# Kernel optimization log

Measured on AMD Instinct MI355X. Metric: run time of the kernel, lower is better.

The kernel has to match this reference:

```python
import jax, jax.numpy as jnp
import numpy as np

V = 25426          # tgt_vocab_size
D = 256            # d_model
H = 8              # heads
DH = 2048          # dim_head (d_ff passed positionally as d_head in source)
INNER = H * DH     # 16384
CLS = V            # cls token id (same value for t1 and t2 in source)
MASK_TOK = V + 2   # mask token id
VT = V + 3         # total embedding vocab


def _pos_encoding(n, d):
    pos = np.arange(n, dtype=np.float32)[:, None]
    div = np.exp(np.arange(0, d, 2, dtype=np.float32) * (-np.log(10000.0) / d))
    pe = np.zeros((n, d), dtype=np.float32)
    pe[:, 0::2] = np.sin(pos * div)
    pe[:, 1::2] = np.cos(pos * div)
    return jnp.asarray(pe)


def _layernorm(x, g, b, eps=1e-5):
    m = x.mean(-1, keepdims=True)
    v = ((x - m) ** 2).mean(-1, keepdims=True)
    return (x - m) / jnp.sqrt(v + eps) * g + b


def _cross_attn(x, ctx, pad_mask, Wq, Wk, Wv, Wo, bo):
    # x: [B,N,D], ctx: [B,M,Dc], pad_mask: [B,M] True = masked
    B, N, _ = x.shape
    M = ctx.shape[1]
    scale = DH ** -0.5
    q = (x @ Wq).reshape(B, N, H, DH)
    k = (ctx @ Wk).reshape(B, M, H, DH)
    v = (ctx @ Wv).reshape(B, M, H, DH)
    sim = jnp.einsum('bihd,bjhd->bhij', q, k) * scale  # [B,H,N,M]
    neg = -jnp.finfo(sim.dtype).max
    sim = jnp.where(pad_mask[:, None, None, :], neg, sim)
    attn = jax.nn.softmax(sim, axis=-1)
    out = jnp.einsum('bhij,bjhd->bihd', attn, v).reshape(B, N, INNER)
    return out @ Wo + bo


def _decoder(x, tgt_pad, src_mask, enc_output, p):
    a = _cross_attn(x, x, tgt_pad, p['Wq_s'], p['Wk_s'], p['Wv_s'], p['Wo_s'], p['bo_s'])
    x = _layernorm(x + a, p['g1'], p['be1'])
    a = _cross_attn(x, enc_output, src_mask, p['Wq_c'], p['Wk_c'], p['Wv_c'], p['Wo_c'], p['bo_c'])
    x = _layernorm(x + a, p['g2'], p['be2'])
    f = jax.nn.gelu(x @ p['W1'] + p['b1'], approximate=False) @ p['W2'] + p['b2']
    x = _layernorm(x + f, p['g3'], p['be3'])
    return x


def setup_inputs() -> dict:
    key = jax.random.key(0)
    ks = jax.random.split(key, 32)
    B, S, L = 2, 1024, 767
    d = {
        'src_input_id': jax.random.randint(ks[0], (B, S), 0, V),
        'tgt_input_id_t1': jax.random.randint(ks[1], (B, L), 0, V),
        'tgt_input_id_t2': jax.random.randint(ks[2], (B, L), 0, V),
        'original_lens': jax.random.randint(ks[3], (B,), 1, L),
        'enc_output': jax.random.normal(ks[4], (B, S, D), dtype=jnp.float32),
    }
    emb = jax.random.normal(ks[5], (VT, D), dtype=jnp.float32) * 0.02
    d['token_emb'] = emb.at[0].set(0.0)  # padding_idx=0
    s = 0.02
    d['Wq_s'] = jax.random.normal(ks[6], (D, INNER)) * s
    d['Wk_s'] = jax.random.normal(ks[7], (D, INNER)) * s
    d['Wv_s'] = jax.random.normal(ks[8], (D, INNER)) * s
    d['Wo_s'] = jax.random.normal(ks[9], (INNER, D)) * s
    d['bo_s'] = jnp.zeros((D,), jnp.float32)
    d['Wq_c'] = jax.random.normal(ks[10], (D, INNER)) * s
    d['Wk_c'] = jax.random.normal(ks[11], (D, INNER)) * s
    d['Wv_c'] = jax.random.normal(ks[12], (D, INNER)) * s
    d['Wo_c'] = jax.random.normal(ks[13], (INNER, D)) * s
    d['bo_c'] = jnp.zeros((D,), jnp.float32)
    d['W1'] = jax.random.normal(ks[14], (D, D)) * s  # Mlp hidden collapses to D (source bug)
    d['b1'] = jnp.zeros((D,), jnp.float32)
    d['W2'] = jax.random.normal(ks[15], (D, D)) * s
    d['b2'] = jnp.zeros((D,), jnp.float32)
    for i, n in enumerate(['g1', 'g2', 'g3']):
        d[n] = jnp.ones((D,), jnp.float32)
    for n in ['be1', 'be2', 'be3']:
        d[n] = jnp.zeros((D,), jnp.float32)
    d['Wfc'] = jax.random.normal(ks[16], (D, V)) * s
    d['bfc'] = jnp.zeros((V,), jnp.float32)
    return d


def reference(src_input_id, tgt_input_id_t1, tgt_input_id_t2, original_lens,
              enc_output, token_emb,
              Wq_s, Wk_s, Wv_s, Wo_s, bo_s,
              Wq_c, Wk_c, Wv_c, Wo_c, bo_c,
              W1, b1, W2, b2, g1, be1, g2, be2, g3, be3, Wfc, bfc):
    p = dict(Wq_s=Wq_s, Wk_s=Wk_s, Wv_s=Wv_s, Wo_s=Wo_s, bo_s=bo_s,
             Wq_c=Wq_c, Wk_c=Wk_c, Wv_c=Wv_c, Wo_c=Wo_c, bo_c=bo_c,
             W1=W1, b1=b1, W2=W2, b2=b2, g1=g1, be1=be1, g2=g2, be2=be2, g3=g3, be3=be3)
    B = tgt_input_id_t1.shape[0]
    cls = jnp.full((B, 1), CLS, dtype=tgt_input_id_t1.dtype)
    t1 = jnp.concatenate([cls, tgt_input_id_t1], axis=1)
    t2 = jnp.concatenate([cls, tgt_input_id_t2], axis=1)
    tgt = jnp.concatenate([t1, t2], axis=1)          # [B, T]
    tgt_pad = tgt == 0
    src_mask = src_input_id == 0
    # generate=True path: mask positions where id==mask_token or id==0
    tgt_mask = (tgt == MASK_TOK) | (tgt == 0)
    tgt_ids = jnp.where(tgt_mask, MASK_TOK, tgt)
    x = token_emb[tgt_ids]                            # [B, T, D]
    pe = _pos_encoding(x.shape[1], D)
    x = 2.0 * x + pe[None, :, :]                      # prepare_tokens: x + (x + pe), faithful to source
    x = _decoder(x, tgt_pad, src_mask, enc_output, p)
    logits = x @ Wfc + bfc
    return logits[:, 1:, :], x[:, 0, :]
```

## Files before the change

### kernel.cpp

```cpp
#include <hip/hip_runtime.h>
#include <hip/hip_bf16.h>
#include <float.h>
#include <math.h>

#define BB 2
#define SS 1024
#define LL 767
#define TT 1536
#define DD 256
#define HH 8
#define DHD 2048
#define INNER_ 16384
#define VV 25426
#define VPAD 25472
#define CLS_TOK 25426
#define MASK_TOKEN 25428
#define ROWS (BB*TT)
#define SROWS (BB*SS)

typedef __attribute__((ext_vector_type(8))) __bf16 bf16x8;
typedef __attribute__((ext_vector_type(4))) float f32x4;

__device__ __forceinline__ unsigned short f2bu(float f) {
    union { float f; unsigned u; } v; v.f = f;
    unsigned r = v.u + 0x7fff + ((v.u >> 16) & 1);
    return (unsigned short)(r >> 16);
}
__device__ __forceinline__ float bu2f(unsigned short u) {
    union { unsigned u; float f; } v; v.u = ((unsigned)u) << 16;
    return v.f;
}

__device__ __forceinline__ void gload16(const void* g, void* l) {
    __builtin_amdgcn_global_load_lds(
        (const __attribute__((address_space(1))) void*)g,
        (__attribute__((address_space(3))) void*)l, 16, 0, 0);
}


__global__ __launch_bounds__(256) void embed_kernel(
    const int* __restrict__ t1, const int* __restrict__ t2,
    const float* __restrict__ emb, float* __restrict__ x,
    unsigned short* __restrict__ xb, unsigned char* __restrict__ tgt_pad)
{
    int t = blockIdx.x, b = blockIdx.y, d = threadIdx.x;
    int raw;
    if (t == 0)            raw = CLS_TOK;
    else if (t <= LL)      raw = t1[b * LL + (t - 1)];
    else if (t == LL + 1)  raw = CLS_TOK;
    else                   raw = t2[b * LL + (t - LL - 2)];
    int id = (raw == 0 || raw == MASK_TOKEN) ? MASK_TOKEN : raw;
    int i = d >> 1;
    float ang = (float)t * expf(-0.03597789208f * (float)(2 * i));
    float pe = (d & 1) ? cosf(ang) : sinf(ang);
    float val = 2.f * emb[(long long)id * DD + d] + pe;
    long long idx = ((long long)(b * TT + t)) * DD + d;
    x[idx] = val;
    xb[idx] = f2bu(val);
    if (d == 0) tgt_pad[b * TT + t] = (raw == 0) ? 1 : 0;
}

__global__ __launch_bounds__(256) void masks_kernel(
    const int* __restrict__ src, unsigned char* __restrict__ m, int* __restrict__ rm)
{
    int i = blockIdx.x * 256 + threadIdx.x;
    if (i < SROWS) m[i] = (src[i] == 0) ? 1 : 0;
    if (i < ROWS) {
        int b = i / TT, t = i % TT;
        rm[i] = (t == 0) ? -1 : (b * (TT - 1) + t - 1);
    }
}

__global__ __launch_bounds__(256) void copycls_kernel(
    const float* __restrict__ x, float* __restrict__ out2)
{
    int b = blockIdx.x, d = threadIdx.x;
    out2[b * DD + d] = x[(long long)b * TT * DD + d];
}

__global__ __launch_bounds__(256) void conv_bf16v4(
    const float* __restrict__ in, unsigned short* __restrict__ out)
{
    size_t i = ((size_t)blockIdx.x * 256 + threadIdx.x) * 4;
    float4 v = *reinterpret_cast<const float4*>(in + i);
    ushort4 u;
    u.x = f2bu(v.x); u.y = f2bu(v.y); u.z = f2bu(v.z); u.w = f2bu(v.w);
    *reinterpret_cast<ushort4*>(out + i) = u;
}

__global__ __launch_bounds__(256) void convW6(
    const float* __restrict__ w0, const float* __restrict__ w1,
    const float* __restrict__ w2, const float* __restrict__ w3,
    const float* __restrict__ w4, const float* __restrict__ w5,
    unsigned short* __restrict__ dst)
{
    int seg = blockIdx.y;
    const float* s = seg == 0 ? w0 : seg == 1 ? w1 : seg == 2 ? w2 :
                     seg == 3 ? w3 : seg == 4 ? w4 : w5;
    size_t i = ((size_t)blockIdx.x * 256 + threadIdx.x) * 4;
    float4 v = *reinterpret_cast<const float4*>(s + i);
    ushort4 u;
    u.x = f2bu(v.x); u.y = f2bu(v.y); u.z = f2bu(v.z); u.w = f2bu(v.w);
    *reinterpret_cast<ushort4*>(dst + (size_t)seg * ((size_t)DD * INNER_) + i) = u;
}

__global__ __launch_bounds__(256) void transpose_conv(
    const float* __restrict__ in, unsigned short* __restrict__ out,
    int R, int Cin, int Nout)
{
    __shared__ float t[32][33];
    int k0 = blockIdx.x * 32, n0 = blockIdx.y * 32;
#pragma unroll
    for (int i = 0; i < 4; ++i) {
        int k = k0 + threadIdx.y + i * 8;
        int n = n0 + threadIdx.x;
        t[threadIdx.y + i * 8][threadIdx.x] = (n < Cin) ? in[(size_t)k * Cin + n] : 0.f;
    }
    __syncthreads();
#pragma unroll
    for (int i = 0; i < 4; ++i) {
        int n = n0 + threadIdx.y + i * 8;
        int k = k0 + threadIdx.x;
        out[(size_t)n * R + k] = f2bu(t[threadIdx.x][threadIdx.y + i * 8]);
    }
}

template<int STORE, int SPLITK>
__global__ __launch_bounds__(256) void gemm_bt(
    const unsigned short* __restrict__ A, int lda,
    const unsigned short* __restrict__ B, int ldb,
    void* __restrict__ Cv, int ldc,
    int M, int N, int K, float alpha, int zs,
    long long sAb, long long sAh, long long sBb, long long sBh,
    long long sCb, long long sCh,
    const float* __restrict__ bias, const int* __restrict__ rowmap)
{
    __shared__ unsigned short As[8192];
    __shared__ unsigned short Bs[8192];
    const int tid = threadIdx.x;
    const int w = tid >> 6, l = tid & 63;
    const int m0 = blockIdx.x * 128, n0 = blockIdx.y * 128;

    constexpr int KSH = (SPLITK == 8) ? 3 : (SPLITK == 4) ? 2 : (SPLITK == 2) ? 1 : 0;
    const int kidx = blockIdx.z & (SPLITK - 1);
    const int zfull = blockIdx.z >> KSH;
    const int zb = zfull >> zs;
    const int zh = zfull - (zb << zs);
    const int kc = K / SPLITK;
    const int kbeg = kidx * kc, kend = kbeg + kc;
    A += zb * sAb + zh * sAh;
    B += zb * sBb + zh * sBh;
    const long long czoff = zb * sCb + zh * sCh;

    const int wr = (w >> 1) << 6, wc = (w & 1) << 6;
    const int lrow = l & 15, lk = l >> 4;

    const int sro = (w << 3) + (l >> 3);
    const int sko = (((l & 7) ^ (l >> 3)) << 3);
    const int ldst = (w << 10) + (l << 4);

    f32x4 acc[4][4];
#pragma unroll
    for (int mi = 0; mi < 4; ++mi)
#pragma unroll
        for (int ni = 0; ni < 4; ++ni)
            acc[mi][ni] = (f32x4){0.f, 0.f, 0.f, 0.f};

    for (int kt = kbeg; kt < kend; kt += 64) {
#pragma unroll
        for (int j = 0; j < 4; ++j)
            gload16(A + (size_t)(m0 + sro + j * 32) * lda + kt + sko,
                    (char*)As + (j << 12) + ldst);
#pragma unroll
        for (int j = 0; j < 4; ++j)
            gload16(B + (size_t)(n0 + sro + j * 32) * ldb + kt + sko,
                    (char*)Bs + (j << 12) + ldst);
        __syncthreads();

#pragma unroll
        for (int kk = 0; kk < 2; ++kk) {
            const int slot = (kk << 2) + lk;
            bf16x8 af[4], bfr[4];
#pragma unroll
            for (int mi = 0; mi < 4; ++mi) {
                int ra = wr + (mi << 4) + lrow;
                af[mi] = *reinterpret_cast<const bf16x8*>(
                    (const char*)As + (ra << 7) + ((slot ^ (ra & 7)) << 4));
            }
#pragma unroll
            for (int ni = 0; ni < 4; ++ni) {
                int rb = wc + (ni << 4) + lrow;
                bfr[ni] = *reinterpret_cast<const bf16x8*>(
                    (const char*)Bs + (rb << 7) + ((slot ^ (rb & 7)) << 4));
            }
#pragma unroll
            for (int mi = 0; mi < 4; ++mi)
#pragma unroll
                for (int ni = 0; ni < 4; ++ni)
                    acc[mi][ni] = __builtin_amdgcn_mfma_f32_16x16x32_bf16(
                        af[mi], bfr[ni], acc[mi][ni], 0, 0, 0);
        }
        __syncthreads();
    }

    if (STORE == 0) {
        unsigned short* C = (unsigned short*)Cv + czoff;
#pragma unroll
        for (int mi = 0; mi < 4; ++mi) {
            int r = m0 + wr + (mi << 4) + (lk << 2);
#pragma unroll
            for (int ni = 0; ni < 4; ++ni) {
                int c = n0 + wc + (ni << 4) + lrow;
#pragma unroll
                for (int q = 0; q < 4; ++q)
                    C[(size_t)(r + q) * ldc + c] = f2bu(acc[mi][ni][q] * alpha);
            }
        }
    } else if (STORE == 1) {
        unsigned short* C = (unsigned short*)Cv + czoff;
#pragma unroll
        for (int ni = 0; ni < 4; ++ni) {
            int c = n0 + wc + (ni << 4) + lrow;
#pragma unroll
            for (int mi = 0; mi < 4; ++mi) {
                int r = m0 + wr + (mi << 4) + (lk << 2);
                ushort4 u;
                u.x = f2bu(acc[mi][ni][0] * alpha);
                u.y = f2bu(acc[mi][ni][1] * alpha);
                u.z = f2bu(acc[mi][ni][2] * alpha);
                u.w = f2bu(acc[mi][ni][3] * alpha);
                *reinterpret_cast<ushort4*>(&C[(size_t)c * ldc + r]) = u;
            }
        }
    } else if (STORE == 2) {
        float* C = (float*)Cv;
#pragma unroll
        for (int mi = 0; mi < 4; ++mi) {
            int r = m0 + wr + (mi << 4) + (lk << 2);
#pragma unroll
            for (int q = 0; q < 4; ++q) {
                int rm = rowmap[r + q];
                if (rm < 0) continue;
#pragma unroll
                for (int ni = 0; ni < 4; ++ni) {
                    int c = n0 + wc + (ni << 4) + lrow;
                    if (c < N) C[(size_t)rm * ldc + c] = acc[mi][ni][q] * alpha + bias[c];
                }
            }
        }
    } else if (STORE == 3) {
        float* C = (float*)Cv + czoff;
#pragma unroll
        for (int mi = 0; mi < 4; ++mi) {
            int r = m0 + wr + (mi << 4) + (lk << 2);
#pragma unroll
            for (int ni = 0; ni < 4; ++ni) {
                int c = n0 + wc + (ni << 4) + lrow;
#pragma unroll
                for (int q = 0; q < 4; ++q)
                    atomicAdd(&C[(size_t)(r + q) * ldc + c], acc[mi][ni][q] * alpha);
            }
        }
    } else if (STORE == 4) {
        unsigned short* C = (unsigned short*)Cv + czoff;
#pragma unroll
        for (int mi = 0; mi < 4; ++mi) {
            int r = m0 + wr + (mi << 4) + (lk << 2);
#pragma unroll
            for (int ni = 0; ni < 4; ++ni) {
                int c = n0 + wc + (ni << 4) + lrow;
#pragma unroll
                for (int q = 0; q < 4; ++q) {
                    float v = acc[mi][ni][q] * alpha + bias[c];
                    v = 0.5f * v * (1.f + erff(v * 0.70710678118f));
                    C[(size_t)(r + q) * ldc + c] = f2bu(v);
                }
            }
        }
    } else if (STORE == 5) {
        float* C = (float*)Cv + czoff;
#pragma unroll
        for (int mi = 0; mi < 4; ++mi) {
            int r = m0 + wr + (mi << 4) + (lk << 2);
#pragma unroll
            for (int ni = 0; ni < 4; ++ni) {
                int c = n0 + wc + (ni << 4) + lrow;
#pragma unroll
                for (int q = 0; q < 4; ++q)
                    C[(size_t)(r + q) * ldc + c] = acc[mi][ni][q] * alpha;
            }
        }
    } else if (STORE == 6) {
        unsigned short* C = (unsigned short*)Cv + czoff;
        const unsigned char* mrow =
            (const unsigned char*)rowmap + (size_t)(zfull >> zs) * N;
        float* rsum = (float*)bias;
        float rpart[4][4];
#pragma unroll
        for (int mi = 0; mi < 4; ++mi)
#pragma unroll
            for (int q = 0; q < 4; ++q) rpart[mi][q] = 0.f;
#pragma unroll
        for (int mi = 0; mi < 4; ++mi) {
            int r = m0 + wr + (mi << 4) + (lk << 2);
#pragma unroll
            for (int ni = 0; ni < 4; ++ni) {
                int c = n0 + wc + (ni << 4) + lrow;
                bool msk = mrow[c] != 0;
#pragma unroll
                for (int q = 0; q < 4; ++q) {
                    float e = msk ? 0.f : expf(acc[mi][ni][q] * alpha);
                    C[(size_t)(r + q) * ldc + c] = f2bu(e);
                    rpart[mi][q] += e;
                }
            }
        }
#pragma unroll
        for (int mi = 0; mi < 4; ++mi)
#pragma unroll
            for (int q = 0; q < 4; ++q) {
                float s = rpart[mi][q];
                s += __shfl_xor(s, 1);
                s += __shfl_xor(s, 2);
                s += __shfl_xor(s, 4);
                s += __shfl_xor(s, 8);
                if (lrow == 0) {
                    int r = m0 + wr + (mi << 4) + (lk << 2) + q;
                    atomicAdd(&rsum[(size_t)zfull * M + r], s);
                }
            }
    } else {
        float* C = (float*)Cv + czoff;
#pragma unroll
        for (int mi = 0; mi < 4; ++mi) {
            int r = m0 + wr + (mi << 4) + (lk << 2);
#pragma unroll
            for (int q = 0; q < 4; ++q) {
                float rinv = 1.f / bias[(size_t)zfull * M + r + q];
#pragma unroll
                for (int ni = 0; ni < 4; ++ni) {
                    int c = n0 + wc + (ni << 4) + lrow;
                    atomicAdd(&C[(size_t)(r + q) * ldc + c], acc[mi][ni][q] * rinv);
                }
            }
        }
    }
}

__global__ __launch_bounds__(256) void ln_kernel(
    float* __restrict__ x, const float* __restrict__ a,
    const float* __restrict__ abias,
    const float* __restrict__ g, const float* __restrict__ be,
    unsigned short* __restrict__ xb)
{
    __shared__ float red[4];
    const long long r = blockIdx.x;
    const int d = threadIdx.x;
    const long long idx = r * DD + d;
    float v = x[idx] + a[idx];
    if (abias) v += abias[d];

    float s = v;
#pragma unroll
    for (int off = 32; off > 0; off >>= 1) s += __shfl_down(s, off);
    if ((d & 63) == 0) red[d >> 6] = s;
    __syncthreads();
    float mean = (red[0] + red[1] + red[2] + red[3]) * (1.f / DD);
    __syncthreads();

    float df = v - mean;
    float s2 = df * df;
#pragma unroll
    for (int off = 32; off > 0; off >>= 1) s2 += __shfl_down(s2, off);
    if ((d & 63) == 0) red[d >> 6] = s2;
    __syncthreads();
    float var = (red[0] + red[1] + red[2] + red[3]) * (1.f / DD);

    float o = df / sqrtf(var + 1e-5f) * g[d] + be[d];
    x[idx] = o;
    xb[idx] = f2bu(o);
}

extern "C" void kernel_launch(void* const* d_in, const int* in_sizes, int n_in,
                              void* d_out, int out_size, void* d_ws, size_t ws_size,
                              hipStream_t stream)
{
    const int*   src_ids = (const int*)d_in[0];
    const int*   t1      = (const int*)d_in[1];
    const int*   t2      = (const int*)d_in[2];
    const float* enc  = (const float*)d_in[4];
    const float* emb  = (const float*)d_in[5];
    const float* Wq_s = (const float*)d_in[6];
    const float* Wk_s = (const float*)d_in[7];
    const float* Wv_s = (const float*)d_in[8];
    const float* Wo_s = (const float*)d_in[9];
    const float* bo_s = (const float*)d_in[10];
    const float* Wq_c = (const float*)d_in[11];
    const float* Wk_c = (const float*)d_in[12];
    const float* Wv_c = (const float*)d_in[13];
    const float* Wo_c = (const float*)d_in[14];
    const float* bo_c = (const float*)d_in[15];
    const float* W1   = (const float*)d_in[16];
    const float* b1   = (const float*)d_in[17];
    const float* W2   = (const float*)d_in[18];
    const float* b2   = (const float*)d_in[19];
    const float* g1   = (const float*)d_in[20];
    const float* g2v  = (const float*)d_in[21];
    const float* g3   = (const float*)d_in[22];
    const float* be1  = (const float*)d_in[23];
    const float* be2  = (const float*)d_in[24];
    const float* be3  = (const float*)d_in[25];
    const float* Wfc  = (const float*)d_in[26];
    const float* bfc  = (const float*)d_in[27];

    char* p = (char*)d_ws;
    float* x    = (float*)p;           p += (size_t)ROWS * DD * 4;
    float* aout = (float*)p;           p += (size_t)ROWS * DD * 4;
    float* rsum = (float*)p;           p += (size_t)16 * TT * 4;
    unsigned short* h1b  = (unsigned short*)p; p += (size_t)ROWS * DD * 2;
    unsigned short* xb   = (unsigned short*)p; p += (size_t)ROWS * DD * 2;
    unsigned short* encb = (unsigned short*)p; p += (size_t)SROWS * DD * 2;
    unsigned short* Wqb_s = (unsigned short*)p; p += (size_t)DD * INNER_ * 2;
    unsigned short* Wkb_s = (unsigned short*)p; p += (size_t)DD * INNER_ * 2;
    unsigned short* Wvb_s = (unsigned short*)p; p += (size_t)DD * INNER_ * 2;
    unsigned short* Wqb_c = (unsigned short*)p; p += (size_t)DD * INNER_ * 2;
    unsigned short* Wkb_c = (unsigned short*)p; p += (size_t)DD * INNER_ * 2;
    unsigned short* Wvb_c = (unsigned short*)p; p += (size_t)DD * INNER_ * 2;
    unsigned short* WoTs  = (unsigned short*)p; p += (size_t)DD * INNER_ * 2;
    unsigned short* WoTc  = (unsigned short*)p; p += (size_t)DD * INNER_ * 2;
    unsigned short* WfcT  = (unsigned short*)p; p += (size_t)VPAD * DD * 2;
    unsigned short* W1Tb  = (unsigned short*)p; p += (size_t)DD * DD * 2;
    unsigned short* W2Tb  = (unsigned short*)p; p += (size_t)DD * DD * 2;
    unsigned short* MtNb  = (unsigned short*)p; p += (size_t)4 * 524288 * 2;
    unsigned char* tgtpad = (unsigned char*)p; p += ROWS;
    unsigned char* srcpad = (unsigned char*)p; p += SROWS;
    p = (char*)(((size_t)p + 15) & ~(size_t)15);
    int* rowmap = (int*)p;             p += (size_t)ROWS * 4;

    unsigned short* Mtb_s = MtNb;
    unsigned short* Ntb_s = MtNb + 524288;
    unsigned short* Mtb_c = MtNb + 2 * 524288;
    unsigned short* Ntb_c = MtNb + 3 * 524288;

    unsigned short* ob = (unsigned short*)d_out;
    unsigned short* simS = ob;
    unsigned short* Pb   = ob + 37748736;
    unsigned short* YTb  = Pb + 6291456;
    float* MNacc = (float*)d_out;

    const size_t accset = (size_t)ROWS * DD * 4 + (size_t)16 * TT * 4;
    const long long WBLK = 4194304;

    embed_kernel<<<dim3(TT, BB), 256, 0, stream>>>(t1, t2, emb, x, xb, tgtpad);
    masks_kernel<<<dim3(ROWS / 256), 256, 0, stream>>>(src_ids, srcpad, rowmap);
    conv_bf16v4<<<dim3((SROWS * DD) / 1024), 256, 0, stream>>>(enc, encb);

    dim3 tcb(32, 8);
    convW6<<<dim3((DD * INNER_) / 1024, 6), 256, 0, stream>>>(
        Wq_s, Wk_s, Wv_s, Wq_c, Wk_c, Wv_c, Wqb_s);
    transpose_conv<<<dim3(512, 8), tcb, 0, stream>>>(Wo_s, WoTs, INNER_, DD, DD);
    transpose_conv<<<dim3(512, 8), tcb, 0, stream>>>(Wo_c, WoTc, INNER_, DD, DD);
    transpose_conv<<<dim3(8, VPAD / 32), tcb, 0, stream>>>(Wfc, WfcT, DD, VV, VPAD);
    transpose_conv<<<dim3(8, 8), tcb, 0, stream>>>(W1, W1Tb, DD, DD, DD);
    transpose_conv<<<dim3(8, 8), tcb, 0, stream>>>(W2, W2Tb, DD, DD, DD);

    const float scale = 0.022097086912079608f;
    const long long Z0 = 0;

    hipMemsetAsync(MNacc, 0, (size_t)4 * 524288 * 4, stream);
    gemm_bt<3, 4><<<dim3(2, 2, 64), 256, 0, stream>>>(
        Wkb_s, INNER_, Wqb_s, INNER_, MNacc, 256, 256, 256, DHD, 1.f, 3,
        3 * WBLK, 2048, 3 * WBLK, 2048, 2 * 524288, 65536, nullptr, nullptr);
    gemm_bt<3, 4><<<dim3(2, 2, 64), 256, 0, stream>>>(
        WoTs, INNER_, Wvb_s, INNER_, MNacc + 524288, 2048, 256, 256, DHD, 1.f, 3,
        WBLK, 2048, 3 * WBLK, 2048, 2 * 524288, 256, nullptr, nullptr);
    conv_bf16v4<<<dim3((4 * 524288) / 1024), 256, 0, stream>>>(MNacc, MtNb);

    hipMemsetAsync(aout, 0, accset, stream);
    gemm_bt<0, 1><<<dim3(24, 2, 8), 256, 0, stream>>>(
        xb, DD, Mtb_s, DD, Pb, DD, ROWS, DD, DD, 1.f, 3,
        Z0, Z0, Z0, 65536, Z0, 786432, nullptr, nullptr);
    gemm_bt<1, 1><<<dim3(24, 2, 8), 256, 0, stream>>>(
        xb, DD, Ntb_s, 2048, YTb, ROWS, ROWS, DD, DD, 1.f, 3,
        Z0, Z0, Z0, 256, Z0, 786432, nullptr, nullptr);
    gemm_bt<6, 1><<<dim3(12, 12, 16), 256, 0, stream>>>(
        Pb, DD, xb, DD, simS, TT, TT, TT, DD, scale, 3,
        393216, 786432, 393216, Z0,
        18874368, 2359296, (const float*)rsum, (const int*)tgtpad);
    gemm_bt<7, 2><<<dim3(12, 2, 32), 256, 0, stream>>>(
        simS, TT, YTb, ROWS, aout, DD, TT, DD, TT, 1.f, 3,
        18874368, 2359296, 1536, 786432,
        393216, Z0, rsum, nullptr);
    ln_kernel<<<dim3(ROWS), 256, 0, stream>>>(x, aout, bo_s, g1, be1, xb);

    hipMemsetAsync(aout, 0, accset, stream);
    gemm_bt<0, 1><<<dim3(24, 2, 8), 256, 0, stream>>>(
        xb, DD, Mtb_c, DD, Pb, DD, ROWS, DD, DD, 1.f, 3,
        Z0, Z0, Z0, 65536, Z0, 786432, nullptr, nullptr);
    gemm_bt<1, 1><<<dim3(16, 2, 8), 256, 0, stream>>>(
        encb, DD, Ntb_c, 2048, YTb, SROWS, SROWS, DD, DD, 1.f, 3,
        Z0, Z0, Z0, 256, Z0, 524288, nullptr, nullptr);
    gemm_bt<6, 1><<<dim3(12, 8, 16), 256, 0, stream>>>(
        Pb, DD, encb, DD, simS, SS, TT, SS, DD, scale, 3,
        393216, 786432, 262144, Z0,
        12582912, 1572864, (const float*)rsum, (const int*)srcpad);
    gemm_bt<7, 2><<<dim3(12, 2, 32), 256, 0, stream>>>(
        simS, SS, YTb, SROWS, aout, DD, TT, DD, SS, 1.f, 3,
        12582912, 1572864, 1024, 524288,
        393216, Z0, rsum, nullptr);
    ln_kernel<<<dim3(ROWS), 256, 0, stream>>>(x, aout, bo_c, g2v, be2, xb);

    gemm_bt<4, 1><<<dim3(24, 2, 1), 256, 0, stream>>>(
        xb, DD, W1Tb, DD, h1b, DD, ROWS, DD, DD, 1.f, 0,
        Z0, Z0, Z0, Z0, Z0, Z0, b1, nullptr);
    gemm_bt<5, 1><<<dim3(24, 2, 1), 256, 0, stream>>>(
        h1b, DD, W2Tb, DD, aout, DD, ROWS, DD, DD, 1.f, 0,
        Z0, Z0, Z0, Z0, Z0, Z0, nullptr, nullptr);
    ln_kernel<<<dim3(ROWS), 256, 0, stream>>>(x, aout, b2, g3, be3, xb);

    gemm_bt<2, 1><<<dim3(24, VPAD / 128, 1), 256, 0, stream>>>(
        xb, DD, WfcT, DD, d_out, VV, ROWS, VV, DD, 1.f, 0,
        Z0, Z0, Z0, Z0, Z0, Z0, bfc, rowmap);

    copycls_kernel<<<dim3(BB), 256, 0, stream>>>(
        x, (float*)d_out + (long long)BB * (TT - 1) * VV);
}
```

Measured before the change: 603.4 us.

## Replace atomic head reduction in attention PV with per-head stores and LN-side sum

The attention output GEMM no longer splits K and atomically accumulates all heads into one fp32 buffer. Each head now plain-stores its normalized output into a separate per-head slice of a scratch buffer. A new layernorm kernel sums the 8 head slices, adds bias and the residual, then normalizes. This removes atomic contention and the large output memset, at the cost of writing and re-reading 8x more fp32 data and giving up split-K parallelism (half the grid).

```diff
diff --git a/kernel.cpp b/kernel.cpp
--- a/kernel.cpp
+++ b/kernel.cpp
@@ -329,7 +329,7 @@
                     atomicAdd(&rsum[(size_t)zfull * M + r], s);
                 }
             }
-    } else {
+    } else if (STORE == 7) {
         float* C = (float*)Cv + czoff;
 #pragma unroll
         for (int mi = 0; mi < 4; ++mi) {
@@ -344,7 +344,60 @@
                 }
             }
         }
+    } else {
+        float* C = (float*)Cv + czoff;
+#pragma unroll
+        for (int mi = 0; mi < 4; ++mi) {
+            int r = m0 + wr + (mi << 4) + (lk << 2);
+#pragma unroll
+            for (int q = 0; q < 4; ++q) {
+                float rinv = 1.f / bias[(size_t)zfull * M + r + q];
+#pragma unroll
+                for (int ni = 0; ni < 4; ++ni) {
+                    int c = n0 + wc + (ni << 4) + lrow;
+                    C[(size_t)(r + q) * ldc + c] = acc[mi][ni][q] * rinv;
+                }
+            }
+        }
     }
+}
+
+__global__ __launch_bounds__(256) void ln8_kernel(
+    float* __restrict__ x, const float* __restrict__ Oh,
+    const float* __restrict__ abias,
+    const float* __restrict__ g, const float* __restrict__ be,
+    unsigned short* __restrict__ xb)
+{
+    __shared__ float red[4];
+    const int r = blockIdx.x;
+    const int b = (r >= 1536) ? 1 : 0;
+    const int t = r - b * 1536;
+    const int d = threadIdx.x;
+    const long long idx = (long long)r * DD + d;
+    float v = x[idx] + abias[d];
+    const float* op = Oh + ((size_t)b * 8 * 1536 + t) * 256 + d;
+#pragma unroll
+    for (int h = 0; h < 8; ++h) v += op[(size_t)h * 1536 * 256];
+
+    float s = v;
+#pragma unroll
+    for (int off = 32; off > 0; off >>= 1) s += __shfl_down(s, off);
+    if ((d & 63) == 0) red[d >> 6] = s;
+    __syncthreads();
+    float mean = (red[0] + red[1] + red[2] + red[3]) * (1.f / DD);
+    __syncthreads();
+
+    float df = v - mean;
+    float s2 = df * df;
+#pragma unroll
+    for (int off = 32; off > 0; off >>= 1) s2 += __shfl_down(s2, off);
+    if ((d & 63) == 0) red[d >> 6] = s2;
+    __syncthreads();
+    float var = (red[0] + red[1] + red[2] + red[3]) * (1.f / DD);
+
+    float o = df / sqrtf(var + 1e-5f) * g[d] + be[d];
+    x[idx] = o;
+    xb[idx] = f2bu(o);
 }
 
 __global__ __launch_bounds__(256) void ln_kernel(
@@ -446,9 +499,9 @@
     unsigned short* simS = ob;
     unsigned short* Pb   = ob + 37748736;
     unsigned short* YTb  = Pb + 6291456;
+    float* Oh = (float*)((char*)d_out + 100663296);
     float* MNacc = (float*)d_out;
 
-    const size_t accset = (size_t)ROWS * DD * 4 + (size_t)16 * TT * 4;
     const long long WBLK = 4194304;
 
     embed_kernel<<<dim3(TT, BB), 256, 0, stream>>>(t1, t2, emb, x, xb, tgtpad);
@@ -476,7 +529,7 @@
         WBLK, 2048, 3 * WBLK, 2048, 2 * 524288, 256, nullptr, nullptr);
     conv_bf16v4<<<dim3((4 * 524288) / 1024), 256, 0, stream>>>(MNacc, MtNb);
 
-    hipMemsetAsync(aout, 0, accset, stream);
+    hipMemsetAsync(rsum, 0, (size_t)16 * TT * 4, stream);
     gemm_bt<0, 1><<<dim3(24, 2, 8), 256, 0, stream>>>(
         xb, DD, Mtb_s, DD, Pb, DD, ROWS, DD, DD, 1.f, 3,
         Z0, Z0, Z0, 65536, Z0, 786432, nullptr, nullptr);
@@ -487,13 +540,13 @@
         Pb, DD, xb, DD, simS, TT, TT, TT, DD, scale, 3,
         393216, 786432, 393216, Z0,
         18874368, 2359296, (const float*)rsum, (const int*)tgtpad);
-    gemm_bt<7, 2><<<dim3(12, 2, 32), 256, 0, stream>>>(
-        simS, TT, YTb, ROWS, aout, DD, TT, DD, TT, 1.f, 3,
+    gemm_bt<8, 1><<<dim3(12, 2, 16), 256, 0, stream>>>(
+        simS, TT, YTb, ROWS, Oh, DD, TT, DD, TT, 1.f, 3,
         18874368, 2359296, 1536, 786432,
-        393216, Z0, rsum, nullptr);
-    ln_kernel<<<dim3(ROWS), 256, 0, stream>>>(x, aout, bo_s, g1, be1, xb);
-
-    hipMemsetAsync(aout, 0, accset, stream);
+        3145728, 393216, rsum, nullptr);
+    ln8_kernel<<<dim3(ROWS), 256, 0, stream>>>(x, Oh, bo_s, g1, be1, xb);
+
+    hipMemsetAsync(rsum, 0, (size_t)16 * TT * 4, stream);
     gemm_bt<0, 1><<<dim3(24, 2, 8), 256, 0, stream>>>(
         xb, DD, Mtb_c, DD, Pb, DD, ROWS, DD, DD, 1.f, 3,
         Z0, Z0, Z0, 65536, Z0, 786432, nullptr, nullptr);
@@ -504,11 +557,11 @@
         Pb, DD, encb, DD, simS, SS, TT, SS, DD, scale, 3,
         393216, 786432, 262144, Z0,
         12582912, 1572864, (const float*)rsum, (const int*)srcpad);
-    gemm_bt<7, 2><<<dim3(12, 2, 32), 256, 0, stream>>>(
-        simS, SS, YTb, SROWS, aout, DD, TT, DD, SS, 1.f, 3,
+    gemm_bt<8, 1><<<dim3(12, 2, 16), 256, 0, stream>>>(
+        simS, SS, YTb, SROWS, Oh, DD, TT, DD, SS, 1.f, 3,
         12582912, 1572864, 1024, 524288,
-        393216, Z0, rsum, nullptr);
-    ln_kernel<<<dim3(ROWS), 256, 0, stream>>>(x, aout, bo_c, g2v, be2, xb);
+        3145728, 393216, rsum, nullptr);
+    ln8_kernel<<<dim3(ROWS), 256, 0, stream>>>(x, Oh, bo_c, g2v, be2, xb);
 
     gemm_bt<4, 1><<<dim3(24, 2, 1), 256, 0, stream>>>(
         xb, DD, W1Tb, DD, h1b, DD, ROWS, DD, DD, 1.f, 0,
```

Measured after the change: 544.0 us. -9.8%, faster.
